# Performance work log

Measured on AMD Instinct MI355X. Metric: run time of the kernel, lower is better.

## Reference

```python
import jax, jax.numpy as jnp
import numpy as np

BOUND = 2.0  # class attr `bound`


def _interp1d(fac, v):
    """Emulates F.grid_sample(fac[1,R,D,1], coords with x=0, align_corners=True,
    padding_mode='border') as a 1-D linear interpolation.
    fac: (rank, D) table, v: (N,) coords nominally in [-1, 1].
    Returns (rank, N)."""
    D = fac.shape[1]
    pos = jnp.clip((v + 1.0) * 0.5 * (D - 1), 0.0, float(D - 1))
    i0 = jnp.clip(jnp.floor(pos).astype(jnp.int32), 0, D - 2)
    w = pos - i0  # in [0, 1]
    return fac[:, i0] * (1.0 - w) + fac[:, i0 + 1] * w


def setup_inputs() -> dict:
    key = jax.random.key(0)
    ks = jax.random.split(key, 11)
    N = 4194304
    rank = 5
    f32 = jnp.float32
    xyz = jax.random.normal(ks[0], (N, 3), f32)            # world coords
    rgb = jax.random.uniform(ks[1], (N, 3), f32)           # colors in [0,1]
    # CP factors (fac_i = learned residual + identity init, passed combined)
    fac0 = jax.random.normal(ks[2], (12, rank), f32) * 0.1  # Linear(rank->12) weight
    fac1 = jax.random.normal(ks[3], (rank, 8), f32) * 0.1   # grid_W axis (x coord)
    fac2 = jax.random.normal(ks[4], (rank, 16), f32) * 0.1  # grid_Z axis (y coord)
    fac3 = jax.random.normal(ks[5], (rank, 16), f32) * 0.1  # grid_Y axis (z coord)
    fac4 = jax.random.normal(ks[6], (rank, 16), f32) * 0.1  # grid_X axis (gray)
    w1 = jax.random.normal(ks[7], (8, 3), f32) * 0.5
    b1 = jnp.zeros((8,), f32)
    w2 = jax.random.normal(ks[8], (1, 8), f32) * 0.5
    b2 = jnp.zeros((1,), f32)
    return dict(xyz=xyz, rgb=rgb, fac0=fac0, fac1=fac1, fac2=fac2,
                fac3=fac3, fac4=fac4, w1=w1, b1=b1, w2=w2, b2=b2)


def reference(xyz, rgb, fac0, fac1, fac2, fac3, fac4, w1, b1, w2, b2):
    sh = xyz.shape
    xyz = xyz.reshape(-1, 3) / BOUND
    rgb = rgb.reshape(-1, 3)
    # learned gray: tanh(2 * MLP(rgb)) in (-1, 1)
    h = jax.nn.relu(rgb @ w1.T + b1)
    gray = jnp.tanh(2.0 * (h @ w2.T + b2))[:, 0]  # (N,)
    # product of four 1-D interpolated CP factor lookups -> (rank, N)
    coef = (_interp1d(fac1, xyz[:, 0])
            * _interp1d(fac2, xyz[:, 1])
            * _interp1d(fac3, xyz[:, 2])
            * _interp1d(fac4, gray))
    mat = coef.T @ fac0.T  # (N, 12): Linear(rank->12, no bias)
    return mat.reshape(*sh[:-1], 3, 4)
```

## Files before the change

kernel.cpp:

```cpp
#include <hip/hip_runtime.h>


constexpr int RANK = 5;

__device__ __forceinline__ void interp_lds(const float* __restrict__ s, int D,
                                           float v, float* la) {
    const float dm1 = (float)(D - 1);
    float pos = (v + 1.0f) * 0.5f * dm1;
    pos = fminf(fmaxf(pos, 0.0f), dm1);
    int i0 = (int)pos;
    if (i0 > D - 2) i0 = D - 2;
    float w = pos - (float)i0;
#pragma unroll
    for (int r = 0; r < RANK; ++r) {
        float a = s[r * D + i0];
        float b = s[r * D + i0 + 1];
        la[r] = fmaf(w, b - a, a);
    }
}

__global__ __launch_bounds__(256) void bg_kernel(
    const float* __restrict__ xyz, const float* __restrict__ rgb,
    const float* __restrict__ fac0, const float* __restrict__ fac1,
    const float* __restrict__ fac2, const float* __restrict__ fac3,
    const float* __restrict__ fac4, const float* __restrict__ w1,
    const float* __restrict__ b1, const float* __restrict__ w2,
    const float* __restrict__ b2, float* __restrict__ out, int n, int n4)
{
    __shared__ float s1[RANK * 8];
    __shared__ float s2[RANK * 16];
    __shared__ float s3[RANK * 16];
    __shared__ float s4[RANK * 16];
    const int tid = threadIdx.x;
    if (tid < RANK * 8) s1[tid] = fac1[tid];
    if (tid < RANK * 16) {
        s2[tid] = fac2[tid];
        s3[tid] = fac3[tid];
        s4[tid] = fac4[tid];
    }
    __syncthreads();

    const int t = blockIdx.x * 256 + tid;
    if (t >= n4) return;
    const int p0 = 4 * t;

    float px[4], py[4], pz[4], pr[4], pg[4], pb[4];
    int cnt;
    if (p0 + 4 <= n) {
        cnt = 4;
        const float4* xyz4 = (const float4*)xyz;
        const float4* rgb4 = (const float4*)rgb;
        float4 xa = xyz4[3 * t + 0], xb = xyz4[3 * t + 1], xc = xyz4[3 * t + 2];
        float4 ra = rgb4[3 * t + 0], rb = rgb4[3 * t + 1], rc = rgb4[3 * t + 2];
        px[0] = xa.x; px[1] = xa.w; px[2] = xb.z; px[3] = xc.y;
        py[0] = xa.y; py[1] = xb.x; py[2] = xb.w; py[3] = xc.z;
        pz[0] = xa.z; pz[1] = xb.y; pz[2] = xc.x; pz[3] = xc.w;
        pr[0] = ra.x; pr[1] = ra.w; pr[2] = rb.z; pr[3] = rc.y;
        pg[0] = ra.y; pg[1] = rb.x; pg[2] = rb.w; pg[3] = rc.z;
        pb[0] = ra.z; pb[1] = rb.y; pb[2] = rc.x; pb[3] = rc.w;
    } else {
        cnt = n - p0;
#pragma unroll
        for (int q = 0; q < 4; ++q) {
            int p = p0 + q; if (p > n - 1) p = n - 1;
            px[q] = xyz[3 * p + 0]; py[q] = xyz[3 * p + 1]; pz[q] = xyz[3 * p + 2];
            pr[q] = rgb[3 * p + 0]; pg[q] = rgb[3 * p + 1]; pb[q] = rgb[3 * p + 2];
        }
    }

    float4* out4 = (float4*)out;
#pragma unroll
    for (int q = 0; q < 4; ++q) {
        if (q >= cnt) break;
        const float x = px[q] * 0.5f;
        const float y = py[q] * 0.5f;
        const float z = pz[q] * 0.5f;

        float acc = b2[0];
#pragma unroll
        for (int k = 0; k < 8; ++k) {
            float hk = fmaf(pr[q], w1[3 * k + 0],
                       fmaf(pg[q], w1[3 * k + 1],
                       fmaf(pb[q], w1[3 * k + 2], b1[k])));
            hk = fmaxf(hk, 0.0f);
            acc = fmaf(hk, w2[k], acc);
        }
        float e = __expf(4.0f * acc);
        float gray = 1.0f - 2.0f * __builtin_amdgcn_rcpf(e + 1.0f);

        float l1[RANK], l2[RANK], l3[RANK], l4[RANK];
        interp_lds(s1, 8,  x,    l1);
        interp_lds(s2, 16, y,    l2);
        interp_lds(s3, 16, z,    l3);
        interp_lds(s4, 16, gray, l4);

        float coef[RANK];
#pragma unroll
        for (int r = 0; r < RANK; ++r)
            coef[r] = (l1[r] * l2[r]) * (l3[r] * l4[r]);

        float o[12];
#pragma unroll
        for (int j = 0; j < 12; ++j) {
            float s = coef[0] * fac0[j * RANK + 0];
#pragma unroll
            for (int r = 1; r < RANK; ++r)
                s = fmaf(coef[r], fac0[j * RANK + r], s);
            o[j] = s;
        }
        const int ob = 12 * t + 3 * q;
        out4[ob + 0] = make_float4(o[0], o[1], o[2],  o[3]);
        out4[ob + 1] = make_float4(o[4], o[5], o[6],  o[7]);
        out4[ob + 2] = make_float4(o[8], o[9], o[10], o[11]);
    }
}

extern "C" void kernel_launch(void* const* d_in, const int* in_sizes, int n_in,
                              void* d_out, int out_size, void* d_ws, size_t ws_size,
                              hipStream_t stream)
{
    const float* xyz  = (const float*)d_in[0];
    const float* rgb  = (const float*)d_in[1];
    const float* fac0 = (const float*)d_in[2];
    const float* fac1 = (const float*)d_in[3];
    const float* fac2 = (const float*)d_in[4];
    const float* fac3 = (const float*)d_in[5];
    const float* fac4 = (const float*)d_in[6];
    const float* w1   = (const float*)d_in[7];
    const float* b1   = (const float*)d_in[8];
    const float* w2   = (const float*)d_in[9];
    const float* b2   = (const float*)d_in[10];
    float* out = (float*)d_out;

    const int n  = in_sizes[0] / 3;
    const int n4 = (n + 3) / 4;
    const int blocks = (n4 + 255) / 256;
    bg_kernel<<<blocks, 256, 0, stream>>>(xyz, rgb, fac0, fac1, fac2, fac3, fac4,
                                          w1, b1, w2, b2, out, n, n4);
}
```

Before: 364.7 us.

## Stage inputs and outputs through LDS for fully coalesced global access

Each block of 256 threads now handles 512 points. It loads the xyz and rgb slices into shared memory with contiguous float4 reads, then computes each point from LDS. Results go into a padded (stride 13) LDS buffer and are written back as contiguous float4 stores. Before, each thread read 3 strided float4s and wrote 12 per 4 points, so wavefront accesses were strided. The change adds about 26 KB of LDS per block, extra barriers and integer divide-by-3 indexing, which may lower occupancy.

```diff
diff --git a/kernel.cpp b/kernel.cpp
--- a/kernel.cpp
+++ b/kernel.cpp
@@ -25,12 +25,14 @@
     const float* __restrict__ fac2, const float* __restrict__ fac3,
     const float* __restrict__ fac4, const float* __restrict__ w1,
     const float* __restrict__ b1, const float* __restrict__ w2,
-    const float* __restrict__ b2, float* __restrict__ out, int n, int n4)
+    const float* __restrict__ b2, float* __restrict__ out, int n)
 {
     __shared__ float s1[RANK * 8];
     __shared__ float s2[RANK * 16];
     __shared__ float s3[RANK * 16];
     __shared__ float s4[RANK * 16];
+    __shared__ float stage[13 * 512];
+
     const int tid = threadIdx.x;
     if (tid < RANK * 8) s1[tid] = fac1[tid];
     if (tid < RANK * 16) {
@@ -38,80 +40,105 @@
         s3[tid] = fac3[tid];
         s4[tid] = fac4[tid];
     }
+
+    const int pbase  = blockIdx.x * 512;
+    const int nfloat = n * 3;
+
+    {
+        const float4* gx = (const float4*)xyz;
+        const float4* gr = (const float4*)rgb;
+        float4* st = (float4*)stage;
+        const int fbase4 = (pbase * 3) >> 2;
+#pragma unroll
+        for (int k = tid; k < 384; k += 256) {
+            const int g4 = fbase4 + k;
+            if (4 * g4 + 3 < nfloat) {
+                st[k]       = gx[g4];
+                st[512 + k] = gr[g4];
+            } else {
+                float tx[4], tr[4];
+                for (int c = 0; c < 4; ++c) {
+                    const int fi = 4 * g4 + c;
+                    tx[c] = (fi < nfloat) ? xyz[fi] : 0.0f;
+                    tr[c] = (fi < nfloat) ? rgb[fi] : 0.0f;
+                }
+                st[k]       = make_float4(tx[0], tx[1], tx[2], tx[3]);
+                st[512 + k] = make_float4(tr[0], tr[1], tr[2], tr[3]);
+            }
+        }
+    }
     __syncthreads();
 
-    const int t = blockIdx.x * 256 + tid;
-    if (t >= n4) return;
-    const int p0 = 4 * t;
-
-    float px[4], py[4], pz[4], pr[4], pg[4], pb[4];
-    int cnt;
-    if (p0 + 4 <= n) {
-        cnt = 4;
-        const float4* xyz4 = (const float4*)xyz;
-        const float4* rgb4 = (const float4*)rgb;
-        float4 xa = xyz4[3 * t + 0], xb = xyz4[3 * t + 1], xc = xyz4[3 * t + 2];
-        float4 ra = rgb4[3 * t + 0], rb = rgb4[3 * t + 1], rc = rgb4[3 * t + 2];
-        px[0] = xa.x; px[1] = xa.w; px[2] = xb.z; px[3] = xc.y;
-        py[0] = xa.y; py[1] = xb.x; py[2] = xb.w; py[3] = xc.z;
-        pz[0] = xa.z; pz[1] = xb.y; pz[2] = xc.x; pz[3] = xc.w;
-        pr[0] = ra.x; pr[1] = ra.w; pr[2] = rb.z; pr[3] = rc.y;
-        pg[0] = ra.y; pg[1] = rb.x; pg[2] = rb.w; pg[3] = rc.z;
-        pb[0] = ra.z; pb[1] = rb.y; pb[2] = rc.x; pb[3] = rc.w;
-    } else {
-        cnt = n - p0;
+    float in[2][6];
 #pragma unroll
-        for (int q = 0; q < 4; ++q) {
-            int p = p0 + q; if (p > n - 1) p = n - 1;
-            px[q] = xyz[3 * p + 0]; py[q] = xyz[3 * p + 1]; pz[q] = xyz[3 * p + 2];
-            pr[q] = rgb[3 * p + 0]; pg[q] = rgb[3 * p + 1]; pb[q] = rgb[3 * p + 2];
+    for (int q = 0; q < 2; ++q) {
+        const int pl = tid + 256 * q;
+#pragma unroll
+        for (int c = 0; c < 3; ++c) {
+            in[q][c]     = stage[3 * pl + c];
+            in[q][3 + c] = stage[2048 + 3 * pl + c];
         }
     }
+    __syncthreads();
 
-    float4* out4 = (float4*)out;
 #pragma unroll
-    for (int q = 0; q < 4; ++q) {
-        if (q >= cnt) break;
-        const float x = px[q] * 0.5f;
-        const float y = py[q] * 0.5f;
-        const float z = pz[q] * 0.5f;
+    for (int q = 0; q < 2; ++q) {
+        const int pl = tid + 256 * q;
+        const int p  = pbase + pl;
+        if (p < n) {
+            const float x = in[q][0] * 0.5f;
+            const float y = in[q][1] * 0.5f;
+            const float z = in[q][2] * 0.5f;
+            const float pr = in[q][3], pg = in[q][4], pb = in[q][5];
 
-        float acc = b2[0];
+            float acc = b2[0];
 #pragma unroll
-        for (int k = 0; k < 8; ++k) {
-            float hk = fmaf(pr[q], w1[3 * k + 0],
-                       fmaf(pg[q], w1[3 * k + 1],
-                       fmaf(pb[q], w1[3 * k + 2], b1[k])));
-            hk = fmaxf(hk, 0.0f);
-            acc = fmaf(hk, w2[k], acc);
+            for (int k = 0; k < 8; ++k) {
+                float hk = fmaf(pr, w1[3 * k + 0],
+                           fmaf(pg, w1[3 * k + 1],
+                           fmaf(pb, w1[3 * k + 2], b1[k])));
+                hk = fmaxf(hk, 0.0f);
+                acc = fmaf(hk, w2[k], acc);
+            }
+            const float e = __expf(4.0f * acc);
+            const float gray = 1.0f - 2.0f * __builtin_amdgcn_rcpf(e + 1.0f);
+
+            float l1[RANK], l2[RANK], l3[RANK], l4[RANK];
+            interp_lds(s1, 8,  x,    l1);
+            interp_lds(s2, 16, y,    l2);
+            interp_lds(s3, 16, z,    l3);
+            interp_lds(s4, 16, gray, l4);
+
+            float coef[RANK];
+#pragma unroll
+            for (int r = 0; r < RANK; ++r)
+                coef[r] = (l1[r] * l2[r]) * (l3[r] * l4[r]);
+
+#pragma unroll
+            for (int j = 0; j < 12; ++j) {
+                float s = coef[0] * fac0[j * RANK + 0];
+#pragma unroll
+                for (int r = 1; r < RANK; ++r)
+                    s = fmaf(coef[r], fac0[j * RANK + r], s);
+                stage[13 * pl + j] = s;
+            }
         }
-        float e = __expf(4.0f * acc);
-        float gray = 1.0f - 2.0f * __builtin_amdgcn_rcpf(e + 1.0f);
+    }
+    __syncthreads();
 
-        float l1[RANK], l2[RANK], l3[RANK], l4[RANK];
-        interp_lds(s1, 8,  x,    l1);
-        interp_lds(s2, 16, y,    l2);
-        interp_lds(s3, 16, z,    l3);
-        interp_lds(s4, 16, gray, l4);
-
-        float coef[RANK];
+    float4* o4 = (float4*)out;
+    const int obase4 = pbase * 3;
+    const int olim4  = n * 3;
 #pragma unroll
-        for (int r = 0; r < RANK; ++r)
-            coef[r] = (l1[r] * l2[r]) * (l3[r] * l4[r]);
-
-        float o[12];
-#pragma unroll
-        for (int j = 0; j < 12; ++j) {
-            float s = coef[0] * fac0[j * RANK + 0];
-#pragma unroll
-            for (int r = 1; r < RANK; ++r)
-                s = fmaf(coef[r], fac0[j * RANK + r], s);
-            o[j] = s;
+    for (int i = 0; i < 6; ++i) {
+        const int g = i * 256 + tid;
+        if (obase4 + g < olim4) {
+            const int pl = g / 3;
+            const int k  = g - 3 * pl;
+            const int a  = 13 * pl + 4 * k;
+            o4[obase4 + g] = make_float4(stage[a], stage[a + 1],
+                                         stage[a + 2], stage[a + 3]);
         }
-        const int ob = 12 * t + 3 * q;
-        out4[ob + 0] = make_float4(o[0], o[1], o[2],  o[3]);
-        out4[ob + 1] = make_float4(o[4], o[5], o[6],  o[7]);
-        out4[ob + 2] = make_float4(o[8], o[9], o[10], o[11]);
     }
 }
 
@@ -132,9 +159,8 @@
     const float* b2   = (const float*)d_in[10];
     float* out = (float*)d_out;
 
-    const int n  = in_sizes[0] / 3;
-    const int n4 = (n + 3) / 4;
-    const int blocks = (n4 + 255) / 256;
+    const int n = in_sizes[0] / 3;
+    const int blocks = (n + 511) / 512;
     bg_kernel<<<blocks, 256, 0, stream>>>(xyz, rgb, fac0, fac1, fac2, fac3, fac4,
-                                          w1, b1, w2, b2, out, n, n4);
+                                          w1, b1, w2, b2, out, n);
 }
```

Result: faster. 293.8 us (-19.4%).
